# Optimization experiments

Hardware: AMD Instinct MI355X
Metric: run time of the kernel (lower is better)

## Reference

```python
import jax, jax.numpy as jnp
import numpy as np

HEADS = 4
C_HEAD = 32


def setup_inputs() -> dict:
    key = jax.random.key(0)
    k1, k2, k3 = jax.random.split(key, 3)
    c_in = 256
    c_hid = HEADS * C_HEAD  # 128
    x = jax.random.normal(k1, (4, c_in, 64, 64), dtype=jnp.float32)
    # 1x1 conv weights stored as [out, in]
    w_qkv = jax.random.normal(k2, (3 * c_hid, c_in), dtype=jnp.float32) * (c_in ** -0.5)
    w_out = jax.random.normal(k3, (c_in, c_hid), dtype=jnp.float32) * (c_hid ** -0.5)
    b_out = jnp.zeros((c_in,), dtype=jnp.float32)
    return {"x": x, "w_qkv": w_qkv, "w_out": w_out, "b_out": b_out}


def reference(x, w_qkv, w_out, b_out):
    b, c, h, w = x.shape
    scale = C_HEAD ** -0.5
    # 1x1 conv == channel matmul
    qkv = jnp.einsum('bchw,oc->bohw', x, w_qkv)  # [b, 3*c_hid, h, w]
    q, k, v = jnp.split(qkv, 3, axis=1)
    # b (heads c_head) x y -> b heads c_head (x y)
    def to_heads(t):
        return t.reshape(b, HEADS, C_HEAD, h * w)
    q, k, v = to_heads(q) * scale, to_heads(k), to_heads(v)
    sim = jnp.einsum('bhci,bhcj->bhij', q, k)  # [b, heads, N, N]
    sim = sim - jax.lax.stop_gradient(jnp.max(sim, axis=-1, keepdims=True))
    attn = jax.nn.softmax(sim, axis=-1)
    out = jnp.einsum('bhij,bhcj->bhic', attn, v)  # [b, heads, N, c_head]
    # b h (x y) c -> b (h c) x y
    out = out.transpose(0, 1, 3, 2).reshape(b, HEADS * C_HEAD, h, w)
    out = jnp.einsum('bchw,oc->bohw', out, w_out) + b_out[None, :, None, None]
    return out
```

## Files before the change

### kernel.cpp

```cpp
#include <hip/hip_runtime.h>
#include <hip/hip_bf16.h>
#include <cstdint>
#include <cstddef>


#define NB 4
#define CIN 256
#define CHID 128
#define HEADS 4
#define CHEAD 32
#define NPOS 4096
#define BH 16
#define NTOT 16384
#define QKV_O 384
#define QSCALE_LOG2E 0.2550348229f

typedef float f32x4 __attribute__((ext_vector_type(4)));
typedef float f32x16 __attribute__((ext_vector_type(16)));
typedef short s16x8 __attribute__((ext_vector_type(8)));

static __device__ __forceinline__ unsigned short f2bf(float f) {
    union { float f; unsigned u; } v; v.f = f;
    unsigned r = v.u + 0x7FFFu + ((v.u >> 16) & 1u);
    return (unsigned short)(r >> 16);
}

static __device__ __forceinline__ unsigned int pk2bf(float a, float b) {
    union { __hip_bfloat162 h; unsigned int u; } c;
    c.h = __float22bfloat162_rn(float2{a, b});
    return c.u;
}

static __device__ __forceinline__ void plswap(unsigned& a, unsigned& b) {
#if __has_builtin(__builtin_amdgcn_permlane32_swap)
    auto r = __builtin_amdgcn_permlane32_swap((int)a, (int)b, false, false);
    a = (unsigned)r[0];
    b = (unsigned)r[1];
#else
    int hh = (threadIdx.x >> 5) & 1;
    unsigned ta = (unsigned)__shfl_xor((int)a, 32);
    unsigned tb = (unsigned)__shfl_xor((int)b, 32);
    unsigned na = hh ? tb : a;
    unsigned nb = hh ? b : ta;
    a = na; b = nb;
#endif
}

static __device__ __forceinline__ s16x8 mk8(unsigned a, unsigned b, unsigned c, unsigned d) {
    union { unsigned u[4]; s16x8 v; } x;
    x.u[0] = a; x.u[1] = b; x.u[2] = c; x.u[3] = d;
    return x.v;
}

static __device__ __forceinline__ void async_cp16(const void* g, void* l) {
    __builtin_amdgcn_global_load_lds((const __attribute__((address_space(1))) unsigned int*)g,
                                     (__attribute__((address_space(3))) unsigned int*)l, 16, 0, 0);
}

#define MFMA32(a, b, c) __builtin_amdgcn_mfma_f32_32x32x16_bf16(a, b, c, 0, 0, 0)

#define TBLOCKS (NB * (CIN / 32) * (NPOS / 32))
__global__ __launch_bounds__(256) void k_prep(const float* __restrict__ x,
                                              unsigned short* __restrict__ xT,
                                              const float* __restrict__ wqkv,
                                              const float* __restrict__ wout,
                                              unsigned short* __restrict__ wqkv_bf,
                                              unsigned short* __restrict__ wout_bf) {
    if (blockIdx.x >= TBLOCKS) {
        int i = (blockIdx.x - TBLOCKS) * 256 + threadIdx.x;
        if (i < QKV_O * CIN) wqkv_bf[i] = f2bf(wqkv[i]);
        if (i < CIN * CHID)  wout_bf[i] = f2bf(wout[i]);
        return;
    }
    __shared__ float tile[32][33];
    const int ntiles = NPOS / 32;
    const int ctiles = CIN / 32;
    int b   = blockIdx.x / (ntiles * ctiles);
    int rem = blockIdx.x % (ntiles * ctiles);
    int ct = rem / ntiles;
    int nt = rem % ntiles;
    int c0 = ct * 32, n0 = nt * 32;
    int tc = threadIdx.x / 32;
    int tn = threadIdx.x % 32;
    const float* xb = x + (size_t)b * CIN * NPOS;
#pragma unroll
    for (int it = 0; it < 4; ++it) {
        int c = tc + it * 8;
        tile[c][tn] = xb[(size_t)(c0 + c) * NPOS + n0 + tn];
    }
    __syncthreads();
    unsigned short* xTb = xT + (size_t)b * NPOS * CIN;
#pragma unroll
    for (int it = 0; it < 4; ++it) {
        int n = tc + it * 8;
        xTb[(size_t)(n0 + n) * CIN + c0 + tn] = f2bf(tile[tn][n]);
    }
}

__global__ __launch_bounds__(256, 4) void k_qkv(const unsigned short* __restrict__ wq,
                                                const unsigned short* __restrict__ xT,
                                                unsigned short* __restrict__ Q,
                                                unsigned short* __restrict__ K,
                                                unsigned short* __restrict__ V) {
    __shared__ __align__(16) unsigned char smem[2 * 12288];
    int mt = blockIdx.x % 3;
    int nt = blockIdx.x / 3;
    int wid = threadIdx.x >> 6, lane = threadIdx.x & 63;
    int quad = lane >> 4, low4 = lane & 15;
    int o0 = mt * 128, n0 = nt * 64;
    int lb = lane * 16;

    const unsigned short* srcA0 = wq + (size_t)(o0 + wid * 32 + low4) * CIN + quad * 8;
    const unsigned short* srcA1 = srcA0 + 16 * CIN;
    const unsigned short* srcB  = xT + (size_t)(n0 + wid * 16 + low4) * CIN + quad * 8;
    int dA0 = wid * 2048, dA1 = dA0 + 1024, dB = 8192 + wid * 1024;

    async_cp16(srcA0, smem + dA0 + lb);
    async_cp16(srcA1, smem + dA1 + lb);
    async_cp16(srcB,  smem + dB  + lb);
    __syncthreads();

    f32x4 acc[2][4] = {};
    for (int c = 0; c < 8; ++c) {
        if (c < 7) {
            unsigned char* nxt = smem + ((c + 1) & 1) * 12288;
            async_cp16(srcA0 + (c + 1) * 32, nxt + dA0 + lb);
            async_cp16(srcA1 + (c + 1) * 32, nxt + dA1 + lb);
            async_cp16(srcB  + (c + 1) * 32, nxt + dB  + lb);
        }
        const unsigned char* cur = smem + (c & 1) * 12288;
        s16x8 a0 = *(const s16x8*)(cur + wid * 2048 + lb);
        s16x8 a1 = *(const s16x8*)(cur + wid * 2048 + 1024 + lb);
#pragma unroll
        for (int j = 0; j < 4; ++j) {
            s16x8 bj = *(const s16x8*)(cur + 8192 + j * 1024 + lb);
            acc[0][j] = __builtin_amdgcn_mfma_f32_16x16x32_bf16(a0, bj, acc[0][j], 0, 0, 0);
            acc[1][j] = __builtin_amdgcn_mfma_f32_16x16x32_bf16(a1, bj, acc[1][j], 0, 0, 0);
        }
        __syncthreads();
    }

    if (mt < 2) {
        unsigned short* dst = (mt == 0) ? Q : K;
        float sc = (mt == 0) ? QSCALE_LOG2E : 1.0f;
#pragma unroll
        for (int i = 0; i < 2; ++i) {
            int ol = wid * 32 + i * 16 + quad * 4;
            int head = ol >> 5, ch = ol & 31;
#pragma unroll
            for (int j = 0; j < 4; ++j) {
                int nG = n0 + j * 16 + low4;
                int b = nG >> 12, n = nG & 4095;
                f32x4 v = acc[i][j];
                unsigned long long d =
                    (unsigned long long)pk2bf(v[0] * sc, v[1] * sc) |
                    ((unsigned long long)pk2bf(v[2] * sc, v[3] * sc) << 32);
                *(unsigned long long*)(dst + ((size_t)(b * 4 + head) * NPOS + n) * 32 + ch) = d;
            }
        }
    } else {
        unsigned short* vt = (unsigned short*)smem;
#pragma unroll
        for (int i = 0; i < 2; ++i) {
            int ol = wid * 32 + i * 16 + quad * 4;
#pragma unroll
            for (int j = 0; j < 4; ++j) {
                int col = j * 16 + low4;
#pragma unroll
                for (int r = 0; r < 4; ++r) vt[(ol + r) * 80 + col] = f2bf(acc[i][j][r]);
            }
        }
        __syncthreads();
        int b = n0 >> 12, nbase = n0 & 4095;
#pragma unroll
        for (int rep = 0; rep < 4; ++rep) {
            int idx = rep * 256 + threadIdx.x;
            int row = idx >> 3, c8 = idx & 7;
            s16x8 val = *(const s16x8*)(vt + row * 80 + c8 * 8);
            int head = row >> 5, ch = row & 31;
            *(s16x8*)(V + ((size_t)((b * 4 + head) * 32 + ch)) * NPOS + nbase + c8 * 8) = val;
        }
    }
}

__global__ __launch_bounds__(256, 4) void k_attn(const unsigned short* __restrict__ Q,
                                                 const unsigned short* __restrict__ K,
                                                 const unsigned short* __restrict__ V,
                                                 unsigned short* __restrict__ attnO) {
    __shared__ __align__(16) unsigned char smem[2 * 16384];
    int bh = blockIdx.x & 15;
    int qt = blockIdx.x >> 4;
    int wid = threadIdx.x >> 6;
    int lane = threadIdx.x & 63;
    int q5 = lane & 31, h = lane >> 5;
    int qg = wid & 1, kh = wid >> 1;
    int q0 = qt * 64 + qg * 32;
    int khk = kh * 2048;

    const unsigned short* Qp  = Q + (size_t)bh * NPOS * 32;
    const unsigned short* Kbh = K + (size_t)bh * NPOS * 32;
    const unsigned short* Vbh = V + (size_t)bh * 32 * NPOS;

    s16x8 bq0 = *(const s16x8*)(Qp + (size_t)(q0 + q5) * 32 + h * 8);
    s16x8 bq1 = *(const s16x8*)(Qp + (size_t)(q0 + q5) * 32 + 16 + h * 8);

    const unsigned short* sK = Kbh + (size_t)q5 * 32 + h * 8;
    const unsigned short* sV = Vbh + (size_t)q5 * NPOS + h * 8;

    auto stage = [&](int bufi, int k0) {
        unsigned char* wb = smem + bufi * 16384 + kh * 8192;
        if (qg == 0) {
            const unsigned short* p = sK + (size_t)k0 * 32;
            async_cp16(p,        wb);
            async_cp16(p + 16,   wb + 1024);
            async_cp16(p + 1024, wb + 2048);
            async_cp16(p + 1040, wb + 3072);
        } else {
            const unsigned short* p = sV + k0;
            async_cp16(p,      wb + 4096);
            async_cp16(p + 16, wb + 5120);
            async_cp16(p + 32, wb + 6144);
            async_cp16(p + 48, wb + 7168);
        }
    };

    f32x16 oT = {};
    float lacc0 = 0.0f, lacc1 = 0.0f;
    const int lby = lane * 16;

    stage(0, khk);
    __syncthreads();

#pragma unroll 1
    for (int it = 0; it < 32; ++it) {
        if (it + 1 < 32) stage((it + 1) & 1, khk + (it + 1) * 64);
        const unsigned char* kb = smem + (it & 1) * 16384 + kh * 8192;
#pragma unroll
        for (int t = 0; t < 2; ++t) {
            s16x8 ak0 = *(const s16x8*)(kb + t * 2048 + lby);
            s16x8 ak1 = *(const s16x8*)(kb + t * 2048 + 1024 + lby);
            f32x16 s = {};
            s = MFMA32(ak0, bq0, s);
            s = MFMA32(ak1, bq1, s);
            unsigned p[8];
#pragma unroll
            for (int i = 0; i < 8; ++i) {
                float e0 = __builtin_amdgcn_exp2f(s[2 * i]);
                float e1 = __builtin_amdgcn_exp2f(s[2 * i + 1]);
                if (i & 1) lacc0 += e0 + e1;
                else       lacc1 += e0 + e1;
                p[i] = pk2bf(e0, e1);
            }
            plswap(p[0], p[2]); plswap(p[1], p[3]);
            plswap(p[4], p[6]); plswap(p[5], p[7]);
            s16x8 bplo = mk8(p[0], p[1], p[2], p[3]);
            s16x8 bphi = mk8(p[4], p[5], p[6], p[7]);

            s16x8 av0 = *(const s16x8*)(kb + 4096 + (2 * t) * 1024 + lby);
            s16x8 av1 = *(const s16x8*)(kb + 4096 + (2 * t + 1) * 1024 + lby);
            oT = MFMA32(av0, bplo, oT);
            oT = MFMA32(av1, bphi, oT);
        }
        __syncthreads();
    }

    float lsum = lacc0 + lacc1;
    lsum += __shfl_xor(lsum, 32);

    if (kh) {
        float* area = (float*)(smem + qg * 4352);
#pragma unroll
        for (int j = 0; j < 4; ++j)
            *(f32x4*)(area + j * 256 + lane * 4) =
                f32x4{oT[4 * j], oT[4 * j + 1], oT[4 * j + 2], oT[4 * j + 3]};
        area[1024 + lane] = lsum;
    }
    __syncthreads();
    if (!kh) {
        const float* area = (const float*)(smem + qg * 4352);
        lsum += area[1024 + lane];
        float inv = 1.0f / lsum;
        int b = bh >> 2, head = bh & 3;
        int n = q0 + q5;
        unsigned short* base = attnO + ((size_t)(b * NPOS + n)) * CHID + head * 32 + 4 * h;
#pragma unroll
        for (int j = 0; j < 4; ++j) {
            f32x4 r = *(const f32x4*)(area + j * 256 + lane * 4);
            unsigned long long d =
                (unsigned long long)pk2bf((oT[4 * j] + r[0]) * inv, (oT[4 * j + 1] + r[1]) * inv) |
                ((unsigned long long)pk2bf((oT[4 * j + 2] + r[2]) * inv, (oT[4 * j + 3] + r[3]) * inv) << 32);
            *(unsigned long long*)(base + 8 * j) = d;
        }
    }
}

__global__ __launch_bounds__(256, 4) void k_out(const unsigned short* __restrict__ wo,
                                                const unsigned short* __restrict__ attnO,
                                                const float* __restrict__ bias,
                                                float* __restrict__ out) {
    __shared__ __align__(16) unsigned char smem[2 * 12288];
    int mt = blockIdx.x & 1;
    int nt = blockIdx.x >> 1;
    int wid = threadIdx.x >> 6, lane = threadIdx.x & 63;
    int quad = lane >> 4, low4 = lane & 15;
    int o0 = mt * 128, n0 = nt * 64;
    int lb = lane * 16;

    const unsigned short* srcA0 = wo + (size_t)(o0 + wid * 32 + low4) * CHID + quad * 8;
    const unsigned short* srcA1 = srcA0 + 16 * CHID;
    const unsigned short* srcB  = attnO + (size_t)(n0 + wid * 16 + low4) * CHID + quad * 8;
    int dA0 = wid * 2048, dA1 = dA0 + 1024, dB = 8192 + wid * 1024;

    async_cp16(srcA0, smem + dA0 + lb);
    async_cp16(srcA1, smem + dA1 + lb);
    async_cp16(srcB,  smem + dB  + lb);
    __syncthreads();

    f32x4 acc[2][4] = {};
    for (int c = 0; c < 4; ++c) {
        if (c < 3) {
            unsigned char* nxt = smem + ((c + 1) & 1) * 12288;
            async_cp16(srcA0 + (c + 1) * 32, nxt + dA0 + lb);
            async_cp16(srcA1 + (c + 1) * 32, nxt + dA1 + lb);
            async_cp16(srcB  + (c + 1) * 32, nxt + dB  + lb);
        }
        const unsigned char* cur = smem + (c & 1) * 12288;
        s16x8 a0 = *(const s16x8*)(cur + wid * 2048 + lb);
        s16x8 a1 = *(const s16x8*)(cur + wid * 2048 + 1024 + lb);
#pragma unroll
        for (int j = 0; j < 4; ++j) {
            s16x8 bj = *(const s16x8*)(cur + 8192 + j * 1024 + lb);
            acc[0][j] = __builtin_amdgcn_mfma_f32_16x16x32_bf16(a0, bj, acc[0][j], 0, 0, 0);
            acc[1][j] = __builtin_amdgcn_mfma_f32_16x16x32_bf16(a1, bj, acc[1][j], 0, 0, 0);
        }
        __syncthreads();
    }

#pragma unroll
    for (int i = 0; i < 2; ++i) {
        int ob = o0 + wid * 32 + i * 16 + quad * 4;
#pragma unroll
        for (int j = 0; j < 4; ++j) {
            int nG = n0 + j * 16 + low4;
            int b = nG >> 12, n = nG & 4095;
#pragma unroll
            for (int r = 0; r < 4; ++r) {
                int o = ob + r;
                out[((size_t)(b * CIN + o)) * NPOS + n] = acc[i][j][r] + bias[o];
            }
        }
    }
}

extern "C" void kernel_launch(void* const* d_in, const int* in_sizes, int n_in,
                              void* d_out, int out_size, void* d_ws, size_t ws_size,
                              hipStream_t stream) {
    const float* x    = (const float*)d_in[0];
    const float* wqkv = (const float*)d_in[1];
    const float* wout = (const float*)d_in[2];
    const float* bout = (const float*)d_in[3];
    float* out = (float*)d_out;

    unsigned short* Q       = (unsigned short*)d_ws;
    unsigned short* K       = Q + (size_t)BH * NPOS * 32;
    unsigned short* V       = K + (size_t)BH * NPOS * 32;
    unsigned short* attnO   = V + (size_t)BH * 32 * NPOS;
    unsigned short* xT      = attnO + (size_t)NTOT * CHID;
    unsigned short* wqkv_bf = xT + (size_t)NTOT * CIN;
    unsigned short* wout_bf = wqkv_bf + QKV_O * CIN;

    k_prep<<<TBLOCKS + (QKV_O * CIN + 255) / 256, 256, 0, stream>>>(x, xT, wqkv, wout, wqkv_bf, wout_bf);
    k_qkv<<<3 * (NTOT / 64), 256, 0, stream>>>(wqkv_bf, xT, Q, K, V);
    k_attn<<<(NPOS / 64) * BH, 256, 0, stream>>>(Q, K, V, attnO);
    k_out<<<2 * (NTOT / 64), 256, 0, stream>>>(wout_bf, attnO, bout, out);
}
```

Before: 153.7 us.

## Preload LDS tiles to registers before barrier and interleave QK/PV MFMAs

After: 158.8 us. 3.3% more time.

```diff
diff --git a/kernel.cpp b/kernel.cpp
--- a/kernel.cpp
+++ b/kernel.cpp
@@ -15,6 +15,7 @@
 #define QKV_O 384
 #define QSCALE_LOG2E 0.2550348229f
 
+typedef float f32x2 __attribute__((ext_vector_type(2)));
 typedef float f32x4 __attribute__((ext_vector_type(4)));
 typedef float f32x16 __attribute__((ext_vector_type(16)));
 typedef short s16x8 __attribute__((ext_vector_type(8)));
@@ -225,46 +226,60 @@
     };
 
     f32x16 oT = {};
-    float lacc0 = 0.0f, lacc1 = 0.0f;
+    f32x2 lacc0 = {0.0f, 0.0f}, lacc1 = {0.0f, 0.0f};
     const int lby = lane * 16;
+
+    auto softmax_tile = [&](const f32x16& s, s16x8& bplo, s16x8& bphi) {
+        unsigned p[8];
+#pragma unroll
+        for (int i = 0; i < 8; ++i) {
+            float e0 = __builtin_amdgcn_exp2f(s[2 * i]);
+            float e1 = __builtin_amdgcn_exp2f(s[2 * i + 1]);
+            f32x2 e = {e0, e1};
+            if (i & 1) lacc0 += e;
+            else       lacc1 += e;
+            p[i] = pk2bf(e0, e1);
+        }
+        plswap(p[0], p[2]); plswap(p[1], p[3]);
+        plswap(p[4], p[6]); plswap(p[5], p[7]);
+        bplo = mk8(p[0], p[1], p[2], p[3]);
+        bphi = mk8(p[4], p[5], p[6], p[7]);
+    };
 
     stage(0, khk);
     __syncthreads();
 
 #pragma unroll 1
     for (int it = 0; it < 32; ++it) {
+        const unsigned char* kb = smem + (it & 1) * 16384 + kh * 8192;
+        s16x8 ak00 = *(const s16x8*)(kb + lby);
+        s16x8 ak01 = *(const s16x8*)(kb + 1024 + lby);
+        s16x8 ak10 = *(const s16x8*)(kb + 2048 + lby);
+        s16x8 ak11 = *(const s16x8*)(kb + 3072 + lby);
+        s16x8 av00 = *(const s16x8*)(kb + 4096 + lby);
+        s16x8 av01 = *(const s16x8*)(kb + 5120 + lby);
+        s16x8 av10 = *(const s16x8*)(kb + 6144 + lby);
+        s16x8 av11 = *(const s16x8*)(kb + 7168 + lby);
         if (it + 1 < 32) stage((it + 1) & 1, khk + (it + 1) * 64);
-        const unsigned char* kb = smem + (it & 1) * 16384 + kh * 8192;
-#pragma unroll
-        for (int t = 0; t < 2; ++t) {
-            s16x8 ak0 = *(const s16x8*)(kb + t * 2048 + lby);
-            s16x8 ak1 = *(const s16x8*)(kb + t * 2048 + 1024 + lby);
-            f32x16 s = {};
-            s = MFMA32(ak0, bq0, s);
-            s = MFMA32(ak1, bq1, s);
-            unsigned p[8];
-#pragma unroll
-            for (int i = 0; i < 8; ++i) {
-                float e0 = __builtin_amdgcn_exp2f(s[2 * i]);
-                float e1 = __builtin_amdgcn_exp2f(s[2 * i + 1]);
-                if (i & 1) lacc0 += e0 + e1;
-                else       lacc1 += e0 + e1;
-                p[i] = pk2bf(e0, e1);
-            }
-            plswap(p[0], p[2]); plswap(p[1], p[3]);
-            plswap(p[4], p[6]); plswap(p[5], p[7]);
-            s16x8 bplo = mk8(p[0], p[1], p[2], p[3]);
-            s16x8 bphi = mk8(p[4], p[5], p[6], p[7]);
-
-            s16x8 av0 = *(const s16x8*)(kb + 4096 + (2 * t) * 1024 + lby);
-            s16x8 av1 = *(const s16x8*)(kb + 4096 + (2 * t + 1) * 1024 + lby);
-            oT = MFMA32(av0, bplo, oT);
-            oT = MFMA32(av1, bphi, oT);
-        }
         __syncthreads();
-    }
-
-    float lsum = lacc0 + lacc1;
+
+        f32x16 s0 = {};
+        s0 = MFMA32(ak00, bq0, s0);
+        s0 = MFMA32(ak01, bq1, s0);
+        s16x8 bplo0, bphi0;
+        softmax_tile(s0, bplo0, bphi0);
+        f32x16 s1 = {};
+        s1 = MFMA32(ak10, bq0, s1);
+        s1 = MFMA32(ak11, bq1, s1);
+        oT = MFMA32(av00, bplo0, oT);
+        oT = MFMA32(av01, bphi0, oT);
+        s16x8 bplo1, bphi1;
+        softmax_tile(s1, bplo1, bphi1);
+        oT = MFMA32(av10, bplo1, oT);
+        oT = MFMA32(av11, bphi1, oT);
+    }
+
+    float lsum = lacc0[0] + lacc0[1] + lacc1[0] + lacc1[1];
     lsum += __shfl_xor(lsum, 32);
 
     if (kh) {
```

## Pre-tile K/V into fragment layout and pipeline attention loads with explicit waitcnt

Applied to the files above, without the earlier changes.

Result: no change. 155.7 us (+1.3%).

```diff
diff --git a/kernel.cpp b/kernel.cpp
--- a/kernel.cpp
+++ b/kernel.cpp
@@ -15,6 +15,7 @@
 #define QKV_O 384
 #define QSCALE_LOG2E 0.2550348229f
 
+typedef float f32x2 __attribute__((ext_vector_type(2)));
 typedef float f32x4 __attribute__((ext_vector_type(4)));
 typedef float f32x16 __attribute__((ext_vector_type(16)));
 typedef short s16x8 __attribute__((ext_vector_type(8)));
@@ -59,6 +60,7 @@
 
 #define MFMA32(a, b, c) __builtin_amdgcn_mfma_f32_32x32x16_bf16(a, b, c, 0, 0, 0)
 
+
 #define TBLOCKS (NB * (CIN / 32) * (NPOS / 32))
 __global__ __launch_bounds__(256) void k_prep(const float* __restrict__ x,
                                               unsigned short* __restrict__ xT,
@@ -140,9 +142,7 @@
         __syncthreads();
     }
 
-    if (mt < 2) {
-        unsigned short* dst = (mt == 0) ? Q : K;
-        float sc = (mt == 0) ? QSCALE_LOG2E : 1.0f;
+    if (mt == 0) {
 #pragma unroll
         for (int i = 0; i < 2; ++i) {
             int ol = wid * 32 + i * 16 + quad * 4;
@@ -153,9 +153,29 @@
                 int b = nG >> 12, n = nG & 4095;
                 f32x4 v = acc[i][j];
                 unsigned long long d =
-                    (unsigned long long)pk2bf(v[0] * sc, v[1] * sc) |
-                    ((unsigned long long)pk2bf(v[2] * sc, v[3] * sc) << 32);
-                *(unsigned long long*)(dst + ((size_t)(b * 4 + head) * NPOS + n) * 32 + ch) = d;
+                    (unsigned long long)pk2bf(v[0] * QSCALE_LOG2E, v[1] * QSCALE_LOG2E) |
+                    ((unsigned long long)pk2bf(v[2] * QSCALE_LOG2E, v[3] * QSCALE_LOG2E) << 32);
+                *(unsigned long long*)(Q + ((size_t)(b * 4 + head) * NPOS + n) * 32 + ch) = d;
+            }
+        }
+    } else if (mt == 1) {
+#pragma unroll
+        for (int i = 0; i < 2; ++i) {
+            int ol = wid * 32 + i * 16 + quad * 4;
+            int head = ol >> 5, c0 = ol & 31;
+            int f = c0 >> 4, hh = (c0 >> 3) & 1, j8 = c0 & 7;
+#pragma unroll
+            for (int j = 0; j < 4; ++j) {
+                int nG = n0 + j * 16 + low4;
+                int b = nG >> 12, n = nG & 4095;
+                int bh = b * 4 + head;
+                f32x4 v = acc[i][j];
+                unsigned long long d =
+                    (unsigned long long)pk2bf(v[0], v[1]) |
+                    ((unsigned long long)pk2bf(v[2], v[3]) << 32);
+                size_t addr = (((size_t)bh * 128 + (n >> 5)) * 2 + f) * 512
+                            + (size_t)((((hh << 5) | (n & 31)) << 3) + j8);
+                *(unsigned long long*)(K + addr) = d;
             }
         }
     } else {
@@ -178,7 +198,10 @@
             int row = idx >> 3, c8 = idx & 7;
             s16x8 val = *(const s16x8*)(vt + row * 80 + c8 * 8);
             int head = row >> 5, ch = row & 31;
-            *(s16x8*)(V + ((size_t)((b * 4 + head) * 32 + ch)) * NPOS + nbase + c8 * 8) = val;
+            int bh = b * 4 + head;
+            int nstart = nbase + c8 * 8;
+            int kc = nstart >> 4, hh = (nstart >> 3) & 1;
+            *(s16x8*)(V + ((size_t)(bh * 256 + kc) * 64 + ((hh << 5) | ch)) * 8) = val;
         }
     }
 }
@@ -197,58 +220,65 @@
     int q0 = qt * 64 + qg * 32;
     int khk = kh * 2048;
 
-    const unsigned short* Qp  = Q + (size_t)bh * NPOS * 32;
-    const unsigned short* Kbh = K + (size_t)bh * NPOS * 32;
-    const unsigned short* Vbh = V + (size_t)bh * 32 * NPOS;
+    const unsigned short* Qp = Q + (size_t)bh * NPOS * 32;
 
     s16x8 bq0 = *(const s16x8*)(Qp + (size_t)(q0 + q5) * 32 + h * 8);
     s16x8 bq1 = *(const s16x8*)(Qp + (size_t)(q0 + q5) * 32 + 16 + h * 8);
 
-    const unsigned short* sK = Kbh + (size_t)q5 * 32 + h * 8;
-    const unsigned short* sV = Vbh + (size_t)q5 * NPOS + h * 8;
+    const unsigned short* pKf = K + (size_t)bh * 131072 + lane * 8;
+    const unsigned short* pVf = V + (size_t)bh * 131072 + lane * 8;
 
     auto stage = [&](int bufi, int k0) {
         unsigned char* wb = smem + bufi * 16384 + kh * 8192;
         if (qg == 0) {
-            const unsigned short* p = sK + (size_t)k0 * 32;
+            const unsigned short* p = pKf + (size_t)(k0 >> 5) * 1024;
             async_cp16(p,        wb);
-            async_cp16(p + 16,   wb + 1024);
+            async_cp16(p + 512,  wb + 1024);
             async_cp16(p + 1024, wb + 2048);
-            async_cp16(p + 1040, wb + 3072);
+            async_cp16(p + 1536, wb + 3072);
         } else {
-            const unsigned short* p = sV + k0;
-            async_cp16(p,      wb + 4096);
-            async_cp16(p + 16, wb + 5120);
-            async_cp16(p + 32, wb + 6144);
-            async_cp16(p + 48, wb + 7168);
+            const unsigned short* p = pVf + (size_t)(k0 >> 4) * 512;
+            async_cp16(p,        wb + 4096);
+            async_cp16(p + 512,  wb + 5120);
+            async_cp16(p + 1024, wb + 6144);
+            async_cp16(p + 1536, wb + 7168);
         }
     };
 
     f32x16 oT = {};
-    float lacc0 = 0.0f, lacc1 = 0.0f;
+    f32x2 lacc0 = {0.0f, 0.0f}, lacc1 = {0.0f, 0.0f};
     const int lby = lane * 16;
 
     stage(0, khk);
-    __syncthreads();
 
 #pragma unroll 1
     for (int it = 0; it < 32; ++it) {
-        if (it + 1 < 32) stage((it + 1) & 1, khk + (it + 1) * 64);
+        if (it + 1 < 32) {
+            stage((it + 1) & 1, khk + (it + 1) * 64);
+            asm volatile("s_waitcnt vmcnt(4)" ::: "memory");
+        } else {
+            asm volatile("s_waitcnt vmcnt(0)" ::: "memory");
+        }
+        asm volatile("s_barrier" ::: "memory");
+
         const unsigned char* kb = smem + (it & 1) * 16384 + kh * 8192;
 #pragma unroll
         for (int t = 0; t < 2; ++t) {
             s16x8 ak0 = *(const s16x8*)(kb + t * 2048 + lby);
             s16x8 ak1 = *(const s16x8*)(kb + t * 2048 + 1024 + lby);
             f32x16 s = {};
+            __builtin_amdgcn_s_setprio(1);
             s = MFMA32(ak0, bq0, s);
             s = MFMA32(ak1, bq1, s);
+            __builtin_amdgcn_s_setprio(0);
             unsigned p[8];
 #pragma unroll
             for (int i = 0; i < 8; ++i) {
                 float e0 = __builtin_amdgcn_exp2f(s[2 * i]);
                 float e1 = __builtin_amdgcn_exp2f(s[2 * i + 1]);
-                if (i & 1) lacc0 += e0 + e1;
-                else       lacc1 += e0 + e1;
+                f32x2 e = {e0, e1};
+                if (i & 1) lacc0 += e;
+                else       lacc1 += e;
                 p[i] = pk2bf(e0, e1);
             }
             plswap(p[0], p[2]); plswap(p[1], p[3]);
@@ -258,13 +288,15 @@
 
             s16x8 av0 = *(const s16x8*)(kb + 4096 + (2 * t) * 1024 + lby);
             s16x8 av1 = *(const s16x8*)(kb + 4096 + (2 * t + 1) * 1024 + lby);
+            __builtin_amdgcn_s_setprio(1);
             oT = MFMA32(av0, bplo, oT);
             oT = MFMA32(av1, bphi, oT);
-        }
-        __syncthreads();
-    }
-
-    float lsum = lacc0 + lacc1;
+            __builtin_amdgcn_s_setprio(0);
+        }
+        asm volatile("s_barrier" ::: "memory");
+    }
+
+    float lsum = lacc0[0] + lacc0[1] + lacc1[0] + lacc1[1];
     lsum += __shfl_xor(lsum, 32);
 
     if (kh) {
```
